# Kernel tuning notes

Hardware: AMD Instinct MI355X
Metric: run time of the kernel (lower is better)

## Reference

```python
import jax, jax.numpy as jnp
import numpy as np

N_NODES = 200000
N_EDGES = 1600000
N_GRAPHS = 2000
IN_DIM, W1_DIM, W2_DIM, N_CLASSES = 8, 64, 12, 2


def setup_inputs() -> dict:
    key = jax.random.key(0)
    ks = jax.random.split(key, 9)
    x = jax.random.normal(ks[0], (N_NODES, IN_DIM), dtype=jnp.float32)
    edge_index = jax.random.randint(ks[1], (2, N_EDGES), 0, N_NODES, dtype=jnp.int64)
    batch_index = jnp.sort(jax.random.randint(ks[2], (N_NODES,), 0, N_GRAPHS, dtype=jnp.int64))
    # Glorot-ish scaled params
    W1 = jax.random.normal(ks[3], (IN_DIM, W1_DIM), dtype=jnp.float32) * (1.0 / np.sqrt(IN_DIM))
    b1 = jnp.zeros((W1_DIM,), dtype=jnp.float32)
    W2 = jax.random.normal(ks[4], (W1_DIM, W2_DIM), dtype=jnp.float32) * (1.0 / np.sqrt(W1_DIM))
    b2 = jnp.zeros((W2_DIM,), dtype=jnp.float32)
    Wl = jax.random.normal(ks[5], (W2_DIM, N_CLASSES), dtype=jnp.float32) * (1.0 / np.sqrt(W2_DIM))
    bl = jnp.zeros((N_CLASSES,), dtype=jnp.float32)
    return {"x": x, "edge_index": edge_index, "batch_index": batch_index,
            "W1": W1, "b1": b1, "W2": W2, "b2": b2, "Wl": Wl, "bl": bl}


def _gcn_conv(x, W, b, src, dst, deg_inv_sqrt, n_nodes):
    # x' = D^{-1/2} (A + I) D^{-1/2} X W + b  (self-loops already in src/dst)
    xw = x @ W                                   # [N, out]
    norm = deg_inv_sqrt[src] * deg_inv_sqrt[dst]  # [E+N]
    msg = xw[src] * norm[:, None]                 # edge-wise gather (memory-bound)
    out = jax.ops.segment_sum(msg, dst, num_segments=n_nodes)
    return out + b


def reference(x, edge_index, batch_index, W1, b1, W2, b2, Wl, bl):
    n = x.shape[0]
    loops = jnp.arange(n, dtype=edge_index.dtype)
    src = jnp.concatenate([edge_index[0], loops])
    dst = jnp.concatenate([edge_index[1], loops])
    # degree (with self-loops) on destination nodes, as in PyG gcn_norm
    deg = jax.ops.segment_sum(jnp.ones_like(dst, dtype=x.dtype), dst, num_segments=n)
    deg_inv_sqrt = jax.lax.rsqrt(deg)  # deg >= 1 due to self-loops
    h = jax.nn.relu(_gcn_conv(x, W1, b1, src, dst, deg_inv_sqrt, n))
    h = jax.nn.relu(_gcn_conv(h, W2, b2, src, dst, deg_inv_sqrt, n))
    pooled = jax.ops.segment_max(h, batch_index, num_segments=N_GRAPHS)  # global_max_pool
    logits = pooled @ Wl + bl
    return jax.nn.log_softmax(logits, axis=1)
```

## Files before the change

kernel.cpp:

```cpp
#include <hip/hip_runtime.h>
#include <hip/hip_fp16.h>
#include <stdint.h>


constexpr int IN_DIM = 8;
constexpr int H1 = 64;
constexpr int H2 = 12;
constexpr int NPB = 256;
constexpr int NBK = 782;
constexpr int CAP = 2560;
constexpr int CHUNK = 2048;
constexpr int SLOTS = 16;

__device__ __forceinline__ void acc_row8(float* acc, int4 rv) {
    const __half2* h = (const __half2*)&rv;
#pragma unroll
    for (int q = 0; q < 4; ++q) {
        float2 f = __half22float2(h[q]);
        acc[2 * q] += f.x; acc[2 * q + 1] += f.y;
    }
}

__device__ __forceinline__ void acc_row32(float* acc, int4 ra, int4 rb) {
    const __half2* ha = (const __half2*)&ra;
    const __half2* hb = (const __half2*)&rb;
#pragma unroll
    for (int q = 0; q < 4; ++q) {
        float2 f = __half22float2(ha[q]);
        acc[2 * q] += f.x; acc[2 * q + 1] += f.y;
    }
#pragma unroll
    for (int q = 0; q < 2; ++q) {
        float2 f = __half22float2(hb[q]);
        acc[8 + 2 * q] += f.x; acc[9 + 2 * q] += f.y;
    }
}

__global__ void __launch_bounds__(256) k_binA(
        const int* __restrict__ src, const int* __restrict__ dst,
        uint32_t* __restrict__ pairs, int* __restrict__ bcursor, int ne) {
    __shared__ int s_cnt[NBK];
    __shared__ int s_start[NBK];
    __shared__ int s_gb[NBK];
    __shared__ int s_wsum[4];
    __shared__ uint32_t s_img[CHUNK];
    __shared__ uint16_t s_bkt[CHUNK];
    int t = threadIdx.x;
    int lane = t & 63, wv = t >> 6;
    for (int i = t; i < NBK; i += 256) s_cnt[i] = 0;
    __syncthreads();
    int e0 = blockIdx.x * CHUNK;
    int cntblk = min(CHUNK, ne - e0);
    int rec[8];
#pragma unroll
    for (int i = 0; i < 8; ++i) {
        int e = e0 + i * 256 + t;
        rec[i] = -1;
        if (e < ne) {
            int d = __builtin_nontemporal_load(&dst[e]);
            int b = d >> 8;
            int off = atomicAdd(&s_cnt[b], 1);
            rec[i] = (off << 18) | ((d & 255) << 10) | b;
        }
    }
    __syncthreads();
    int b4 = t * 4;
    int v0 = (b4 < NBK) ? s_cnt[b4] : 0;
    int v1 = (b4 + 1 < NBK) ? s_cnt[b4 + 1] : 0;
    int v2 = (b4 + 2 < NBK) ? s_cnt[b4 + 2] : 0;
    int v3 = (b4 + 3 < NBK) ? s_cnt[b4 + 3] : 0;
    int p1 = v0, p2 = v0 + v1, p3 = v0 + v1 + v2, tot = p3 + v3;
    int inc = tot;
#pragma unroll
    for (int off = 1; off < 64; off <<= 1) {
        int u = __shfl_up(inc, off, 64);
        if (lane >= off) inc += u;
    }
    if (lane == 63) s_wsum[wv] = inc;
    __syncthreads();
    int wpre = 0;
#pragma unroll
    for (int w = 0; w < 3; ++w) wpre += (w < wv) ? s_wsum[w] : 0;
    int ex = wpre + inc - tot;
    if (b4 < NBK)     s_start[b4] = ex;
    if (b4 + 1 < NBK) s_start[b4 + 1] = ex + p1;
    if (b4 + 2 < NBK) s_start[b4 + 2] = ex + p2;
    if (b4 + 3 < NBK) s_start[b4 + 3] = ex + p3;
    for (int b = t; b < NBK; b += 256) {
        int c = s_cnt[b];
        s_gb[b] = (c > 0) ? atomicAdd(&bcursor[b], c) : 0;
    }
    __syncthreads();
#pragma unroll
    for (int i = 0; i < 8; ++i) {
        if (rec[i] < 0) continue;
        int e = e0 + i * 256 + t;
        int b = rec[i] & 1023;
        int dl = (rec[i] >> 10) & 255;
        int off = rec[i] >> 18;
        int pos = s_start[b] + off;
        s_img[pos] = ((uint32_t)dl << 18) | (uint32_t)__builtin_nontemporal_load(&src[e]);
        s_bkt[pos] = (uint16_t)b;
    }
    __syncthreads();
    for (int i = t; i < cntblk; i += 256) {
        int b = s_bkt[i];
        int goff = s_gb[b] + (i - s_start[b]);
        if (goff < CAP) pairs[(size_t)b * CAP + goff] = s_img[i];
    }
}

__global__ void __launch_bounds__(256) k_binB(
        const uint32_t* __restrict__ pairs, const int* __restrict__ bcursor,
        const float* __restrict__ x, int* __restrict__ csr_pad,
        int* __restrict__ csr_ovf, unsigned int* __restrict__ meta,
        float* __restrict__ dis, __half2* __restrict__ xdh, int n) {
    __shared__ int s_hist[NPB];
    __shared__ int s_start[NPB];
    __shared__ int s_wsum[4];
    __shared__ int s_pad[NPB * SLOTS];
    int b = blockIdx.x;
    int t = threadIdx.x;
    int lane = t & 63, wv = t >> 6;
    int cnt = min(bcursor[b], CAP);
    const uint32_t* pb = pairs + (size_t)b * CAP;
    s_hist[t] = 0;
    for (int i = t; i < NPB * SLOTS; i += 256) s_pad[i] = n;
    __syncthreads();
    uint32_t rdl[10];
    uint32_t rsx[10];
#pragma unroll
    for (int r = 0; r < 10; ++r) {
        int i = t + r * 256;
        rdl[r] = 0xFFFFFFFFu;
        if (i < cnt) {
            uint32_t p = __builtin_nontemporal_load(&pb[i]);
            int dl = (int)(p >> 18);
            int off = atomicAdd(&s_hist[dl], 1);
            rdl[r] = ((uint32_t)off << 8) | (uint32_t)dl;
            rsx[r] = p & 0x3FFFFu;
        }
    }
    __syncthreads();
    int v = s_hist[t];
    int inc = v;
#pragma unroll
    for (int off = 1; off < 64; off <<= 1) {
        int u = __shfl_up(inc, off, 64);
        if (lane >= off) inc += u;
    }
    if (lane == 63) s_wsum[wv] = inc;
    __syncthreads();
    int wpre = 0;
#pragma unroll
    for (int w = 0; w < 3; ++w) wpre += (w < wv) ? s_wsum[w] : 0;
    s_start[t] = wpre + inc - v;
    __syncthreads();
    int cb = b * CAP;
    int node = (b << 8) + t;
    if (node < n) {
        int deg = s_hist[t];
        meta[node] = ((unsigned int)deg << 21) | (unsigned int)(cb + s_start[t]);
        float di = rsqrtf((float)(deg + 1));
        dis[node] = di;
        const float4* xi = (const float4*)(x + (size_t)node * IN_DIM);
        float4 a = xi[0], c = xi[1];
        union { __half2 h[4]; int iv[4]; } u;
        u.h[0] = __float22half2_rn(make_float2(a.x * di, a.y * di));
        u.h[1] = __float22half2_rn(make_float2(a.z * di, a.w * di));
        u.h[2] = __float22half2_rn(make_float2(c.x * di, c.y * di));
        u.h[3] = __float22half2_rn(make_float2(c.z * di, c.w * di));
        ((int4*)xdh)[node] = make_int4(u.iv[0], u.iv[1], u.iv[2], u.iv[3]);
    } else if (node == n) {
        ((int4*)xdh)[n] = make_int4(0, 0, 0, 0);
    }
#pragma unroll
    for (int r = 0; r < 10; ++r) {
        if (rdl[r] == 0xFFFFFFFFu) continue;
        int dl = (int)(rdl[r] & 255u);
        int pos = (int)(rdl[r] >> 8);
        int sidx = (int)rsx[r];
        if (pos < SLOTS) s_pad[dl * SLOTS + pos] = sidx;
        else             csr_ovf[cb + s_start[dl] + pos] = sidx;
    }
    __syncthreads();
    for (int i = t; i < NPB * SLOTS / 4; i += 256) {
        int node2 = (b << 8) + (i >> 2);
        if (node2 < n)
            ((int4*)csr_pad)[(size_t)(b << 8) * 4 + i] = ((int4*)s_pad)[i];
    }
}

__global__ void __launch_bounds__(256, 3) k_agg1f(
        const int* __restrict__ csr_pad, const int* __restrict__ csr_ovf,
        const unsigned int* __restrict__ meta, const __half2* __restrict__ xdh,
        const float* __restrict__ dis, const float* __restrict__ W1,
        const float* __restrict__ b1, const float* __restrict__ W2,
        __half2* __restrict__ y2h, int n) {
    int node = blockIdx.x * 256 + threadIdx.x;
    if (node > n) return;
    int4* orow = (int4*)y2h + (size_t)node * 2;
    if (node == n) {
        orow[0] = make_int4(0, 0, 0, 0);
        orow[1] = make_int4(0, 0, 0, 0);
        return;
    }
    const int4* pr = (const int4*)(csr_pad + (size_t)node * SLOTS);
    int4 p0 = pr[0], p1 = pr[1], p2 = pr[2], p3 = pr[3];
    unsigned int m = meta[node];
    const int4* xt = (const int4*)xdh;

    int idx[16] = {p0.x, p0.y, p0.z, p0.w, p1.x, p1.y, p1.z, p1.w,
                   p2.x, p2.y, p2.z, p2.w, p3.x, p3.y, p3.z, p3.w};
    int4 r[17];
    r[0] = xt[node];
#pragma unroll
    for (int i = 0; i < 16; ++i) r[i + 1] = xt[(size_t)idx[i]];
    float acc[8] = {0, 0, 0, 0, 0, 0, 0, 0};
#pragma unroll
    for (int i = 0; i < 17; ++i) acc_row8(acc, r[i]);
    int deg = m >> 21;
    if (deg > SLOTS) {
        int r0 = (int)(m & 0x1FFFFF);
        for (int rr = SLOTS; rr < deg; ++rr) acc_row8(acc, xt[(size_t)csr_ovf[r0 + rr]]);
    }
    float di = dis[node];
    float z[8];
#pragma unroll
    for (int k = 0; k < 8; ++k) z[k] = acc[k] * di;

    float y2[H2];
#pragma unroll
    for (int j = 0; j < H2; ++j) y2[j] = 0.f;
    for (int d = 0; d < H1; ++d) {
        float h = b1[d];
#pragma unroll
        for (int k = 0; k < 8; ++k) h = fmaf(z[k], W1[k * H1 + d], h);
        h = fmaxf(h, 0.f);
#pragma unroll
        for (int j = 0; j < H2; ++j) y2[j] = fmaf(h, W2[d * H2 + j], y2[j]);
    }
    union { __half2 h2v[8]; int iv[8]; } u;
#pragma unroll
    for (int q = 0; q < 6; ++q)
        u.h2v[q] = __float22half2_rn(make_float2(y2[2 * q] * di, y2[2 * q + 1] * di));
    u.h2v[6] = __float22half2_rn(make_float2(0.f, 0.f));
    u.h2v[7] = u.h2v[6];
    orow[0] = make_int4(u.iv[0], u.iv[1], u.iv[2], u.iv[3]);
    orow[1] = make_int4(u.iv[4], u.iv[5], u.iv[6], u.iv[7]);
}

__global__ void __launch_bounds__(256, 3) k_agg2(
        const int* __restrict__ csr_pad, const int* __restrict__ csr_ovf,
        const unsigned int* __restrict__ meta, const __half2* __restrict__ y2h,
        const float* __restrict__ dis, const float* __restrict__ b2,
        const int* __restrict__ batch, unsigned int* __restrict__ pooled, int n) {
    int node = blockIdx.x * 256 + threadIdx.x;
    int lane = threadIdx.x & 63;
    bool active = node < n;
    float v[12] = {0, 0, 0, 0, 0, 0, 0, 0, 0, 0, 0, 0};
    int gid = 0x7fffffff;
    if (active) {
        const int4* pr = (const int4*)(csr_pad + (size_t)node * SLOTS);
        int4 p0 = pr[0], p1 = pr[1], p2 = pr[2], p3 = pr[3];
        unsigned int m = meta[node];
        const int4* yt = (const int4*)y2h;
        int idx[16] = {p0.x, p0.y, p0.z, p0.w, p1.x, p1.y, p1.z, p1.w,
                       p2.x, p2.y, p2.z, p2.w, p3.x, p3.y, p3.z, p3.w};
        float acc[12] = {0, 0, 0, 0, 0, 0, 0, 0, 0, 0, 0, 0};
        int4 ra[9], rb[9];
        ra[0] = yt[(size_t)node * 2];
        rb[0] = yt[(size_t)node * 2 + 1];
#pragma unroll
        for (int i = 0; i < 8; ++i) {
            ra[i + 1] = yt[(size_t)idx[i] * 2];
            rb[i + 1] = yt[(size_t)idx[i] * 2 + 1];
        }
#pragma unroll
        for (int i = 0; i < 9; ++i) acc_row32(acc, ra[i], rb[i]);
#pragma unroll
        for (int i = 0; i < 8; ++i) {
            ra[i] = yt[(size_t)idx[8 + i] * 2];
            rb[i] = yt[(size_t)idx[8 + i] * 2 + 1];
        }
#pragma unroll
        for (int i = 0; i < 8; ++i) acc_row32(acc, ra[i], rb[i]);
        int deg = m >> 21;
        if (deg > SLOTS) {
            int r0 = (int)(m & 0x1FFFFF);
            for (int rr = SLOTS; rr < deg; ++rr) {
                int nb = csr_ovf[r0 + rr];
                acc_row32(acc, yt[(size_t)nb * 2], yt[(size_t)nb * 2 + 1]);
            }
        }
        float di = dis[node];
#pragma unroll
        for (int q = 0; q < 12; ++q) v[q] = fmaxf(fmaf(acc[q], di, b2[q]), 0.f);
        gid = batch[node];
    }
#pragma unroll
    for (int off = 1; off < 64; off <<= 1) {
        int g2 = __shfl_up(gid, off, 64);
        bool merge = (lane >= off) && (g2 == gid);
#pragma unroll
        for (int q = 0; q < 12; ++q) {
            float tv = __shfl_up(v[q], off, 64);
            if (merge) v[q] = fmaxf(v[q], tv);
        }
    }
    int gnext = __shfl_down(gid, 1, 64);
    bool last = (lane == 63) || (gnext != gid);
    if (last && gid != 0x7fffffff) {
        unsigned int* pp = pooled + (size_t)gid * 12;
#pragma unroll
        for (int q = 0; q < 12; ++q) atomicMax(&pp[q], __float_as_uint(v[q]));
    }
}

__global__ void k_head(const unsigned int* __restrict__ pooled,
                       const float* __restrict__ Wl, const float* __restrict__ bl,
                       float* __restrict__ out, int g) {
    int i = blockIdx.x * 256 + threadIdx.x;
    if (i >= g) return;
    float l0 = bl[0], l1 = bl[1];
#pragma unroll
    for (int k = 0; k < H2; ++k) {
        float pv = __uint_as_float(pooled[(size_t)i * 12 + k]);
        l0 = fmaf(pv, Wl[k * 2 + 0], l0);
        l1 = fmaf(pv, Wl[k * 2 + 1], l1);
    }
    float m = fmaxf(l0, l1);
    float lse = m + logf(expf(l0 - m) + expf(l1 - m));
    out[i * 2 + 0] = l0 - lse;
    out[i * 2 + 1] = l1 - lse;
}

extern "C" void kernel_launch(void* const* d_in, const int* in_sizes, int n_in,
                              void* d_out, int out_size, void* d_ws, size_t ws_size,
                              hipStream_t stream) {
    const float* x   = (const float*)d_in[0];
    const int* ei    = (const int*)d_in[1];
    const int* batch = (const int*)d_in[2];
    const float* W1  = (const float*)d_in[3];
    const float* b1  = (const float*)d_in[4];
    const float* W2  = (const float*)d_in[5];
    const float* b2  = (const float*)d_in[6];
    const float* Wl  = (const float*)d_in[7];
    const float* bl  = (const float*)d_in[8];
    float* out = (float*)d_out;

    const int N = in_sizes[0] / IN_DIM;
    const int E = in_sizes[1] / 2;
    const int G = out_size / 2;
    const int* src = ei;
    const int* dst = ei + E;

    auto cdiv = [](long long a, int b) { return (int)((a + b - 1) / b); };

    char* wp = (char*)d_ws;
    auto carve = [&](size_t bytes) {
        char* p = wp;
        wp += (bytes + 63) & ~(size_t)63;
        return p;
    };
    int*          bcursor = (int*)carve(NBK * 4);
    unsigned int* pooled  = (unsigned int*)carve((size_t)G * H2 * 4);
    unsigned int* meta    = (unsigned int*)carve((size_t)N * 4);
    float*        dis     = (float*)carve((size_t)N * 4);
    __half2*      xdh     = (__half2*)carve((size_t)(N + 1) * 16);
    __half2*      y2h     = (__half2*)carve((size_t)(N + 1) * 32);
    uint32_t*     pairs   = (uint32_t*)carve((size_t)NBK * CAP * 4);
    int*          csr_pad = (int*)carve((size_t)N * SLOTS * 4);
    int*          csr_ovf = (int*)carve((size_t)NBK * CAP * 4);

    size_t zspan = (char*)(pooled + (size_t)G * H2) - (char*)bcursor;
    (void)hipMemsetAsync(bcursor, 0, zspan, stream);

    k_binA<<<cdiv(E, CHUNK), 256, 0, stream>>>(src, dst, pairs, bcursor, E);
    k_binB<<<NBK, 256, 0, stream>>>(pairs, bcursor, x, csr_pad, csr_ovf,
                                    meta, dis, xdh, N);

    k_agg1f<<<cdiv((long long)N + 1, 256), 256, 0, stream>>>(
        csr_pad, csr_ovf, meta, xdh, dis, W1, b1, W2, y2h, N);
    k_agg2<<<cdiv(N, 256), 256, 0, stream>>>(csr_pad, csr_ovf, meta, y2h, dis, b2,
                                             batch, pooled, N);
    k_head<<<cdiv(G, 256), 256, 0, stream>>>(pooled, Wl, bl, out, G);
}
```

Before: 174.2 us.

## Fuse both aggregation layers and head into one persistent kernel with grid barriers

Merges the layer-1 aggregation, layer-2 aggregation with max pooling, and the classifier head into one persistent kernel of 768 blocks. Stages are separated by atomic-counter grid barriers, and block 0 computes the head once all blocks have arrived. Zeroing of the pooled buffer moves from the memset into k_binB, so the memset only clears the cursors and barrier counters. This removes two kernel launches and their gaps, but relies on all 768 blocks being co-resident to avoid deadlock, and leaves the head serialized on a single block.

```diff
diff --git a/kernel.cpp b/kernel.cpp
--- a/kernel.cpp
+++ b/kernel.cpp
@@ -11,6 +11,7 @@
 constexpr int CAP = 2560;
 constexpr int CHUNK = 2048;
 constexpr int SLOTS = 16;
+constexpr int AGRID = 768;
 
 __device__ __forceinline__ void acc_row8(float* acc, int4 rv) {
     const __half2* h = (const __half2*)&rv;
@@ -114,7 +115,8 @@
         const uint32_t* __restrict__ pairs, const int* __restrict__ bcursor,
         const float* __restrict__ x, int* __restrict__ csr_pad,
         int* __restrict__ csr_ovf, unsigned int* __restrict__ meta,
-        float* __restrict__ dis, __half2* __restrict__ xdh, int n) {
+        float* __restrict__ dis, __half2* __restrict__ xdh,
+        unsigned int* __restrict__ pooled, int npool, int n) {
     __shared__ int s_hist[NPB];
     __shared__ int s_start[NPB];
     __shared__ int s_wsum[4];
@@ -126,6 +128,10 @@
     const uint32_t* pb = pairs + (size_t)b * CAP;
     s_hist[t] = 0;
     for (int i = t; i < NPB * SLOTS; i += 256) s_pad[i] = n;
+    {
+        int pi = b * 31 + t;
+        if (t < 31 && pi < npool) pooled[pi] = 0u;
+    }
     __syncthreads();
     uint32_t rdl[10];
     uint32_t rsx[10];
@@ -191,148 +197,172 @@
     }
 }
 
-__global__ void __launch_bounds__(256, 3) k_agg1f(
+__global__ void __launch_bounds__(256, 3) k_aggf(
         const int* __restrict__ csr_pad, const int* __restrict__ csr_ovf,
         const unsigned int* __restrict__ meta, const __half2* __restrict__ xdh,
         const float* __restrict__ dis, const float* __restrict__ W1,
         const float* __restrict__ b1, const float* __restrict__ W2,
-        __half2* __restrict__ y2h, int n) {
-    int node = blockIdx.x * 256 + threadIdx.x;
-    if (node > n) return;
-    int4* orow = (int4*)y2h + (size_t)node * 2;
-    if (node == n) {
-        orow[0] = make_int4(0, 0, 0, 0);
-        orow[1] = make_int4(0, 0, 0, 0);
-        return;
-    }
-    const int4* pr = (const int4*)(csr_pad + (size_t)node * SLOTS);
-    int4 p0 = pr[0], p1 = pr[1], p2 = pr[2], p3 = pr[3];
-    unsigned int m = meta[node];
-    const int4* xt = (const int4*)xdh;
-
-    int idx[16] = {p0.x, p0.y, p0.z, p0.w, p1.x, p1.y, p1.z, p1.w,
-                   p2.x, p2.y, p2.z, p2.w, p3.x, p3.y, p3.z, p3.w};
-    int4 r[17];
-    r[0] = xt[node];
-#pragma unroll
-    for (int i = 0; i < 16; ++i) r[i + 1] = xt[(size_t)idx[i]];
-    float acc[8] = {0, 0, 0, 0, 0, 0, 0, 0};
-#pragma unroll
-    for (int i = 0; i < 17; ++i) acc_row8(acc, r[i]);
-    int deg = m >> 21;
-    if (deg > SLOTS) {
-        int r0 = (int)(m & 0x1FFFFF);
-        for (int rr = SLOTS; rr < deg; ++rr) acc_row8(acc, xt[(size_t)csr_ovf[r0 + rr]]);
-    }
-    float di = dis[node];
-    float z[8];
-#pragma unroll
-    for (int k = 0; k < 8; ++k) z[k] = acc[k] * di;
-
-    float y2[H2];
-#pragma unroll
-    for (int j = 0; j < H2; ++j) y2[j] = 0.f;
-    for (int d = 0; d < H1; ++d) {
-        float h = b1[d];
-#pragma unroll
-        for (int k = 0; k < 8; ++k) h = fmaf(z[k], W1[k * H1 + d], h);
-        h = fmaxf(h, 0.f);
-#pragma unroll
-        for (int j = 0; j < H2; ++j) y2[j] = fmaf(h, W2[d * H2 + j], y2[j]);
-    }
-    union { __half2 h2v[8]; int iv[8]; } u;
-#pragma unroll
-    for (int q = 0; q < 6; ++q)
-        u.h2v[q] = __float22half2_rn(make_float2(y2[2 * q] * di, y2[2 * q + 1] * di));
-    u.h2v[6] = __float22half2_rn(make_float2(0.f, 0.f));
-    u.h2v[7] = u.h2v[6];
-    orow[0] = make_int4(u.iv[0], u.iv[1], u.iv[2], u.iv[3]);
-    orow[1] = make_int4(u.iv[4], u.iv[5], u.iv[6], u.iv[7]);
-}
-
-__global__ void __launch_bounds__(256, 3) k_agg2(
-        const int* __restrict__ csr_pad, const int* __restrict__ csr_ovf,
-        const unsigned int* __restrict__ meta, const __half2* __restrict__ y2h,
-        const float* __restrict__ dis, const float* __restrict__ b2,
-        const int* __restrict__ batch, unsigned int* __restrict__ pooled, int n) {
-    int node = blockIdx.x * 256 + threadIdx.x;
-    int lane = threadIdx.x & 63;
-    bool active = node < n;
-    float v[12] = {0, 0, 0, 0, 0, 0, 0, 0, 0, 0, 0, 0};
-    int gid = 0x7fffffff;
-    if (active) {
+        __half2* __restrict__ y2h, const float* __restrict__ b2,
+        const int* __restrict__ batch, unsigned int* __restrict__ pooled,
+        const float* __restrict__ Wl, const float* __restrict__ bl,
+        float* __restrict__ out, unsigned int* __restrict__ bar, int n, int g) {
+    int t = threadIdx.x;
+    int lane = t & 63;
+
+    const int nt1 = (n + 1 + 255) / 256;
+    for (int tile = blockIdx.x; tile < nt1; tile += AGRID) {
+        int node = tile * 256 + t;
+        if (node > n) continue;
+        int4* orow = (int4*)y2h + (size_t)node * 2;
+        if (node == n) {
+            orow[0] = make_int4(0, 0, 0, 0);
+            orow[1] = make_int4(0, 0, 0, 0);
+            continue;
+        }
         const int4* pr = (const int4*)(csr_pad + (size_t)node * SLOTS);
         int4 p0 = pr[0], p1 = pr[1], p2 = pr[2], p3 = pr[3];
         unsigned int m = meta[node];
-        const int4* yt = (const int4*)y2h;
+        const int4* xt = (const int4*)xdh;
+
         int idx[16] = {p0.x, p0.y, p0.z, p0.w, p1.x, p1.y, p1.z, p1.w,
                        p2.x, p2.y, p2.z, p2.w, p3.x, p3.y, p3.z, p3.w};
-        float acc[12] = {0, 0, 0, 0, 0, 0, 0, 0, 0, 0, 0, 0};
-        int4 ra[9], rb[9];
-        ra[0] = yt[(size_t)node * 2];
-        rb[0] = yt[(size_t)node * 2 + 1];
-#pragma unroll
-        for (int i = 0; i < 8; ++i) {
-            ra[i + 1] = yt[(size_t)idx[i] * 2];
-            rb[i + 1] = yt[(size_t)idx[i] * 2 + 1];
-        }
-#pragma unroll
-        for (int i = 0; i < 9; ++i) acc_row32(acc, ra[i], rb[i]);
-#pragma unroll
-        for (int i = 0; i < 8; ++i) {
-            ra[i] = yt[(size_t)idx[8 + i] * 2];
-            rb[i] = yt[(size_t)idx[8 + i] * 2 + 1];
-        }
-#pragma unroll
-        for (int i = 0; i < 8; ++i) acc_row32(acc, ra[i], rb[i]);
+        int4 r[17];
+        r[0] = xt[node];
+#pragma unroll
+        for (int i = 0; i < 16; ++i) r[i + 1] = xt[(size_t)idx[i]];
+        float acc[8] = {0, 0, 0, 0, 0, 0, 0, 0};
+#pragma unroll
+        for (int i = 0; i < 17; ++i) acc_row8(acc, r[i]);
         int deg = m >> 21;
         if (deg > SLOTS) {
             int r0 = (int)(m & 0x1FFFFF);
-            for (int rr = SLOTS; rr < deg; ++rr) {
-                int nb = csr_ovf[r0 + rr];
-                acc_row32(acc, yt[(size_t)nb * 2], yt[(size_t)nb * 2 + 1]);
+            for (int rr = SLOTS; rr < deg; ++rr) acc_row8(acc, xt[(size_t)csr_ovf[r0 + rr]]);
+        }
+        float di = dis[node];
+        float z[8];
+#pragma unroll
+        for (int k = 0; k < 8; ++k) z[k] = acc[k] * di;
+
+        float y2[H2];
+#pragma unroll
+        for (int j = 0; j < H2; ++j) y2[j] = 0.f;
+        for (int d = 0; d < H1; ++d) {
+            float h = b1[d];
+#pragma unroll
+            for (int k = 0; k < 8; ++k) h = fmaf(z[k], W1[k * H1 + d], h);
+            h = fmaxf(h, 0.f);
+#pragma unroll
+            for (int j = 0; j < H2; ++j) y2[j] = fmaf(h, W2[d * H2 + j], y2[j]);
+        }
+        union { __half2 h2v[8]; int iv[8]; } u;
+#pragma unroll
+        for (int q = 0; q < 6; ++q)
+            u.h2v[q] = __float22half2_rn(make_float2(y2[2 * q] * di, y2[2 * q + 1] * di));
+        u.h2v[6] = __float22half2_rn(make_float2(0.f, 0.f));
+        u.h2v[7] = u.h2v[6];
+        orow[0] = make_int4(u.iv[0], u.iv[1], u.iv[2], u.iv[3]);
+        orow[1] = make_int4(u.iv[4], u.iv[5], u.iv[6], u.iv[7]);
+    }
+
+    __syncthreads();
+    if (t == 0) {
+        __threadfence();
+        atomicAdd(&bar[0], 1u);
+        while (atomicAdd(&bar[0], 0u) < (unsigned)AGRID)
+            __builtin_amdgcn_s_sleep(8);
+        __threadfence();
+    }
+    __syncthreads();
+
+    const int nt2 = (n + 255) / 256;
+    for (int tile = blockIdx.x; tile < nt2; tile += AGRID) {
+        int node = tile * 256 + t;
+        bool active = node < n;
+        float v[12] = {0, 0, 0, 0, 0, 0, 0, 0, 0, 0, 0, 0};
+        int gid = 0x7fffffff;
+        if (active) {
+            const int4* pr = (const int4*)(csr_pad + (size_t)node * SLOTS);
+            int4 p0 = pr[0], p1 = pr[1], p2 = pr[2], p3 = pr[3];
+            unsigned int m = meta[node];
+            const int4* yt = (const int4*)y2h;
+            int idx[16] = {p0.x, p0.y, p0.z, p0.w, p1.x, p1.y, p1.z, p1.w,
+                           p2.x, p2.y, p2.z, p2.w, p3.x, p3.y, p3.z, p3.w};
+            float acc[12] = {0, 0, 0, 0, 0, 0, 0, 0, 0, 0, 0, 0};
+            int4 ra[9], rb[9];
+            ra[0] = yt[(size_t)node * 2];
+            rb[0] = yt[(size_t)node * 2 + 1];
+#pragma unroll
+            for (int i = 0; i < 8; ++i) {
+                ra[i + 1] = yt[(size_t)idx[i] * 2];
+                rb[i + 1] = yt[(size_t)idx[i] * 2 + 1];
             }
-        }
-        float di = dis[node];
-#pragma unroll
-        for (int q = 0; q < 12; ++q) v[q] = fmaxf(fmaf(acc[q], di, b2[q]), 0.f);
-        gid = batch[node];
-    }
-#pragma unroll
-    for (int off = 1; off < 64; off <<= 1) {
-        int g2 = __shfl_up(gid, off, 64);
-        bool merge = (lane >= off) && (g2 == gid);
-#pragma unroll
-        for (int q = 0; q < 12; ++q) {
-            float tv = __shfl_up(v[q], off, 64);
-            if (merge) v[q] = fmaxf(v[q], tv);
-        }
-    }
-    int gnext = __shfl_down(gid, 1, 64);
-    bool last = (lane == 63) || (gnext != gid);
-    if (last && gid != 0x7fffffff) {
-        unsigned int* pp = pooled + (size_t)gid * 12;
-#pragma unroll
-        for (int q = 0; q < 12; ++q) atomicMax(&pp[q], __float_as_uint(v[q]));
-    }
-}
-
-__global__ void k_head(const unsigned int* __restrict__ pooled,
-                       const float* __restrict__ Wl, const float* __restrict__ bl,
-                       float* __restrict__ out, int g) {
-    int i = blockIdx.x * 256 + threadIdx.x;
-    if (i >= g) return;
-    float l0 = bl[0], l1 = bl[1];
-#pragma unroll
-    for (int k = 0; k < H2; ++k) {
-        float pv = __uint_as_float(pooled[(size_t)i * 12 + k]);
-        l0 = fmaf(pv, Wl[k * 2 + 0], l0);
-        l1 = fmaf(pv, Wl[k * 2 + 1], l1);
-    }
-    float m = fmaxf(l0, l1);
-    float lse = m + logf(expf(l0 - m) + expf(l1 - m));
-    out[i * 2 + 0] = l0 - lse;
-    out[i * 2 + 1] = l1 - lse;
+#pragma unroll
+            for (int i = 0; i < 9; ++i) acc_row32(acc, ra[i], rb[i]);
+#pragma unroll
+            for (int i = 0; i < 8; ++i) {
+                ra[i] = yt[(size_t)idx[8 + i] * 2];
+                rb[i] = yt[(size_t)idx[8 + i] * 2 + 1];
+            }
+#pragma unroll
+            for (int i = 0; i < 8; ++i) acc_row32(acc, ra[i], rb[i]);
+            int deg = m >> 21;
+            if (deg > SLOTS) {
+                int r0 = (int)(m & 0x1FFFFF);
+                for (int rr = SLOTS; rr < deg; ++rr) {
+                    int nb = csr_ovf[r0 + rr];
+                    acc_row32(acc, yt[(size_t)nb * 2], yt[(size_t)nb * 2 + 1]);
+                }
+            }
+            float di = dis[node];
+#pragma unroll
+            for (int q = 0; q < 12; ++q) v[q] = fmaxf(fmaf(acc[q], di, b2[q]), 0.f);
+            gid = batch[node];
+        }
+#pragma unroll
+        for (int off = 1; off < 64; off <<= 1) {
+            int g2 = __shfl_up(gid, off, 64);
+            bool merge = (lane >= off) && (g2 == gid);
+#pragma unroll
+            for (int q = 0; q < 12; ++q) {
+                float tv = __shfl_up(v[q], off, 64);
+                if (merge) v[q] = fmaxf(v[q], tv);
+            }
+        }
+        int gnext = __shfl_down(gid, 1, 64);
+        bool last = (lane == 63) || (gnext != gid);
+        if (last && gid != 0x7fffffff) {
+            unsigned int* pp = pooled + (size_t)gid * 12;
+#pragma unroll
+            for (int q = 0; q < 12; ++q) atomicMax(&pp[q], __float_as_uint(v[q]));
+        }
+    }
+
+    __syncthreads();
+    if (t == 0) {
+        __threadfence();
+        atomicAdd(&bar[1], 1u);
+    }
+    if (blockIdx.x == 0) {
+        if (t == 0) {
+            while (atomicAdd(&bar[1], 0u) < (unsigned)AGRID)
+                __builtin_amdgcn_s_sleep(8);
+            __threadfence();
+        }
+        __syncthreads();
+        for (int i = t; i < g; i += 256) {
+            float l0 = bl[0], l1 = bl[1];
+#pragma unroll
+            for (int k = 0; k < H2; ++k) {
+                float pv = __uint_as_float(pooled[(size_t)i * 12 + k]);
+                l0 = fmaf(pv, Wl[k * 2 + 0], l0);
+                l1 = fmaf(pv, Wl[k * 2 + 1], l1);
+            }
+            float m = fmaxf(l0, l1);
+            float lse = m + logf(expf(l0 - m) + expf(l1 - m));
+            out[i * 2 + 0] = l0 - lse;
+            out[i * 2 + 1] = l1 - lse;
+        }
+    }
 }
 
 extern "C" void kernel_launch(void* const* d_in, const int* in_sizes, int n_in,
@@ -364,6 +394,7 @@
         return p;
     };
     int*          bcursor = (int*)carve(NBK * 4);
+    unsigned int* bar     = (unsigned int*)carve(2 * 4);
     unsigned int* pooled  = (unsigned int*)carve((size_t)G * H2 * 4);
     unsigned int* meta    = (unsigned int*)carve((size_t)N * 4);
     float*        dis     = (float*)carve((size_t)N * 4);
@@ -373,16 +404,14 @@
     int*          csr_pad = (int*)carve((size_t)N * SLOTS * 4);
     int*          csr_ovf = (int*)carve((size_t)NBK * CAP * 4);
 
-    size_t zspan = (char*)(pooled + (size_t)G * H2) - (char*)bcursor;
+    size_t zspan = (char*)(bar + 2) - (char*)bcursor;
     (void)hipMemsetAsync(bcursor, 0, zspan, stream);
 
     k_binA<<<cdiv(E, CHUNK), 256, 0, stream>>>(src, dst, pairs, bcursor, E);
     k_binB<<<NBK, 256, 0, stream>>>(pairs, bcursor, x, csr_pad, csr_ovf,
-                                    meta, dis, xdh, N);
-
-    k_agg1f<<<cdiv((long long)N + 1, 256), 256, 0, stream>>>(
-        csr_pad, csr_ovf, meta, xdh, dis, W1, b1, W2, y2h, N);
-    k_agg2<<<cdiv(N, 256), 256, 0, stream>>>(csr_pad, csr_ovf, meta, y2h, dis, b2,
-                                             batch, pooled, N);
-    k_head<<<cdiv(G, 256), 256, 0, stream>>>(pooled, Wl, bl, out, G);
-}
+                                    meta, dis, xdh, pooled, G * H2, N);
+
+    k_aggf<<<AGRID, 256, 0, stream>>>(csr_pad, csr_ovf, meta, xdh, dis,
+                                      W1, b1, W2, y2h, b2, batch, pooled,
+                                      Wl, bl, out, bar, N, G);
+}
```

After: 288.6 us. +65.7%, slower.

## Fuse head into agg2 via last-block barrier and fold pooled zeroing

Applied to the files above, without the earlier changes.

Removes the separate head kernel by having the last finishing block of the second aggregation kernel compute logits and log-softmax, using a global atomic counter. Zeroing of the pooled buffer moves into the binning kernel so the memset covers only the small counters. The shared padding prefill is replaced by degree-based masking at write-out. These changes save a kernel launch and some memset and shared-memory stores, at the cost of a serial tail on one block and reliance on fence ordering.

```diff
diff --git a/kernel.cpp b/kernel.cpp
--- a/kernel.cpp
+++ b/kernel.cpp
@@ -114,7 +114,8 @@
         const uint32_t* __restrict__ pairs, const int* __restrict__ bcursor,
         const float* __restrict__ x, int* __restrict__ csr_pad,
         int* __restrict__ csr_ovf, unsigned int* __restrict__ meta,
-        float* __restrict__ dis, __half2* __restrict__ xdh, int n) {
+        float* __restrict__ dis, __half2* __restrict__ xdh,
+        unsigned int* __restrict__ pooled, int npool, int n) {
     __shared__ int s_hist[NPB];
     __shared__ int s_start[NPB];
     __shared__ int s_wsum[4];
@@ -125,7 +126,10 @@
     int cnt = min(bcursor[b], CAP);
     const uint32_t* pb = pairs + (size_t)b * CAP;
     s_hist[t] = 0;
-    for (int i = t; i < NPB * SLOTS; i += 256) s_pad[i] = n;
+    {
+        int pi = b * 31 + t;
+        if (t < 31 && pi < npool) pooled[pi] = 0u;
+    }
     __syncthreads();
     uint32_t rdl[10];
     uint32_t rsx[10];
@@ -185,9 +189,17 @@
     }
     __syncthreads();
     for (int i = t; i < NPB * SLOTS / 4; i += 256) {
-        int node2 = (b << 8) + (i >> 2);
-        if (node2 < n)
-            ((int4*)csr_pad)[(size_t)(b << 8) * 4 + i] = ((int4*)s_pad)[i];
+        int nl = i >> 2;
+        int node2 = (b << 8) + nl;
+        if (node2 >= n) continue;
+        int deg2 = s_hist[nl];
+        int base = (i & 3) * 4;
+        int4 vq = ((int4*)s_pad)[i];
+        vq.x = (base + 0 < deg2) ? vq.x : n;
+        vq.y = (base + 1 < deg2) ? vq.y : n;
+        vq.z = (base + 2 < deg2) ? vq.z : n;
+        vq.w = (base + 3 < deg2) ? vq.w : n;
+        ((int4*)csr_pad)[(size_t)(b << 8) * 4 + i] = vq;
     }
 }
 
@@ -254,7 +266,9 @@
         const int* __restrict__ csr_pad, const int* __restrict__ csr_ovf,
         const unsigned int* __restrict__ meta, const __half2* __restrict__ y2h,
         const float* __restrict__ dis, const float* __restrict__ b2,
-        const int* __restrict__ batch, unsigned int* __restrict__ pooled, int n) {
+        const int* __restrict__ batch, unsigned int* __restrict__ pooled,
+        const float* __restrict__ Wl, const float* __restrict__ bl,
+        float* __restrict__ out, unsigned int* __restrict__ bar, int n, int g) {
     int node = blockIdx.x * 256 + threadIdx.x;
     int lane = threadIdx.x & 63;
     bool active = node < n;
@@ -315,24 +329,31 @@
 #pragma unroll
         for (int q = 0; q < 12; ++q) atomicMax(&pp[q], __float_as_uint(v[q]));
     }
-}
-
-__global__ void k_head(const unsigned int* __restrict__ pooled,
-                       const float* __restrict__ Wl, const float* __restrict__ bl,
-                       float* __restrict__ out, int g) {
-    int i = blockIdx.x * 256 + threadIdx.x;
-    if (i >= g) return;
-    float l0 = bl[0], l1 = bl[1];
-#pragma unroll
-    for (int k = 0; k < H2; ++k) {
-        float pv = __uint_as_float(pooled[(size_t)i * 12 + k]);
-        l0 = fmaf(pv, Wl[k * 2 + 0], l0);
-        l1 = fmaf(pv, Wl[k * 2 + 1], l1);
-    }
-    float m = fmaxf(l0, l1);
-    float lse = m + logf(expf(l0 - m) + expf(l1 - m));
-    out[i * 2 + 0] = l0 - lse;
-    out[i * 2 + 1] = l1 - lse;
+    __shared__ int s_last;
+    __syncthreads();
+    if (threadIdx.x == 0) {
+        __threadfence();
+        unsigned old = atomicAdd(&bar[0], 1u);
+        s_last = (old == (unsigned)(gridDim.x - 1)) ? 1 : 0;
+    }
+    __syncthreads();
+    if (s_last) {
+        if (threadIdx.x == 0) __threadfence();
+        __syncthreads();
+        for (int i = threadIdx.x; i < g; i += 256) {
+            float l0 = bl[0], l1 = bl[1];
+#pragma unroll
+            for (int k = 0; k < H2; ++k) {
+                float pv = __uint_as_float(pooled[(size_t)i * 12 + k]);
+                l0 = fmaf(pv, Wl[k * 2 + 0], l0);
+                l1 = fmaf(pv, Wl[k * 2 + 1], l1);
+            }
+            float m = fmaxf(l0, l1);
+            float lse = m + logf(expf(l0 - m) + expf(l1 - m));
+            out[i * 2 + 0] = l0 - lse;
+            out[i * 2 + 1] = l1 - lse;
+        }
+    }
 }
 
 extern "C" void kernel_launch(void* const* d_in, const int* in_sizes, int n_in,
@@ -364,6 +385,7 @@
         return p;
     };
     int*          bcursor = (int*)carve(NBK * 4);
+    unsigned int* bar     = (unsigned int*)carve(64);
     unsigned int* pooled  = (unsigned int*)carve((size_t)G * H2 * 4);
     unsigned int* meta    = (unsigned int*)carve((size_t)N * 4);
     float*        dis     = (float*)carve((size_t)N * 4);
@@ -373,16 +395,15 @@
     int*          csr_pad = (int*)carve((size_t)N * SLOTS * 4);
     int*          csr_ovf = (int*)carve((size_t)NBK * CAP * 4);
 
-    size_t zspan = (char*)(pooled + (size_t)G * H2) - (char*)bcursor;
+    size_t zspan = (char*)(bar) + 64 - (char*)bcursor;
     (void)hipMemsetAsync(bcursor, 0, zspan, stream);
 
     k_binA<<<cdiv(E, CHUNK), 256, 0, stream>>>(src, dst, pairs, bcursor, E);
     k_binB<<<NBK, 256, 0, stream>>>(pairs, bcursor, x, csr_pad, csr_ovf,
-                                    meta, dis, xdh, N);
+                                    meta, dis, xdh, pooled, G * H2, N);
 
     k_agg1f<<<cdiv((long long)N + 1, 256), 256, 0, stream>>>(
         csr_pad, csr_ovf, meta, xdh, dis, W1, b1, W2, y2h, N);
     k_agg2<<<cdiv(N, 256), 256, 0, stream>>>(csr_pad, csr_ovf, meta, y2h, dis, b2,
-                                             batch, pooled, N);
-    k_head<<<cdiv(G, 256), 256, 0, stream>>>(pooled, Wl, bl, out, G);
-}
+                                             batch, pooled, Wl, bl, out, bar, N, G);
+}
```

New measurement: 197.8 us. 13.5% more time.
